# Kernel optimization log

Hardware: AMD Instinct MI355X
Metric: run time of the kernel (lower is better)

Reference implementation:

```python
import jax, jax.numpy as jnp
import numpy as np

N_MENTIONS = 4096
N_PAIRS = 32768
N_SEGMENTS = 1024  # number of spans (ragged softmax groups)
G_DIM = 3 * 768    # span representation dim (3*embed_dim)
D_IN = 3 * G_DIM + 20
HIDDEN = 150


def setup_inputs() -> dict:
    key = jax.random.key(0)
    ks = jax.random.split(key, 11)
    inp = {
        "g_i": jax.random.normal(ks[0], (N_MENTIONS, G_DIM), jnp.float32),
        "mention_scores": jax.random.normal(ks[1], (N_MENTIONS, 1), jnp.float32),
        "speaker_embed": jax.random.normal(ks[2], (3, 20), jnp.float32) * 0.02,
        "W1": jax.random.normal(ks[3], (D_IN, HIDDEN), jnp.float32) * (1.0 / np.sqrt(D_IN)),
        "b1": jnp.zeros((HIDDEN,), jnp.float32),
        "W2": jax.random.normal(ks[4], (HIDDEN, 1), jnp.float32) * (1.0 / np.sqrt(HIDDEN)),
        "b2": jnp.zeros((1,), jnp.float32),
        "mention_ids": jax.random.randint(ks[5], (N_PAIRS,), 0, N_MENTIONS),
        "antecedent_ids": jax.random.randint(ks[6], (N_PAIRS,), 0, N_MENTIONS),
        "speaker_labels": jax.random.randint(ks[7], (N_PAIRS,), 0, 3),
        "segment_ids": jnp.sort(jax.random.randint(ks[8], (N_PAIRS,), 0, N_SEGMENTS)),
    }
    return inp


def reference(g_i, mention_scores, speaker_embed, W1, b1, W2, b2,
              mention_ids, antecedent_ids, speaker_labels, segment_ids):
    # Gather mention / antecedent span representations. [P, G]
    i_g = g_i[mention_ids]
    j_g = g_i[antecedent_ids]
    phi = speaker_embed[speaker_labels]  # [P, speaker_dim]

    # Pair features: cat(i_g, j_g, i_g*j_g, phi). [P, D_IN]
    pairs = jnp.concatenate([i_g, j_g, i_g * j_g, phi], axis=1)

    # Score MLP: Linear -> ReLU -> Linear(->1). (dropout off in eval)
    h = jax.nn.relu(pairs @ W1 + b1)          # [P, HIDDEN]
    s_ij = (h @ W2 + b2)[:, 0]                # [P]

    # coref score = s_i + s_j + s_ij
    s_i = mention_scores[mention_ids, 0]
    s_j = mention_scores[antecedent_ids, 0]
    scores = s_i + s_j + s_ij                 # [P]

    # Ragged per-span softmax with an appended epsilon logit of 0.0.
    seg_max = jax.ops.segment_max(scores, segment_ids, num_segments=N_SEGMENTS)
    m = jnp.maximum(seg_max, 0.0)             # include epsilon=0 in the max
    e = jnp.exp(scores - m[segment_ids])      # [P]
    eps_e = jnp.exp(-m)                       # [S] exp(0 - m)
    denom = jax.ops.segment_sum(e, segment_ids, num_segments=N_SEGMENTS) + eps_e
    pair_probs = e / denom[segment_ids]       # [P]
    eps_probs = eps_e / denom                 # [S]

    # Flattened: all pair probs followed by the per-span epsilon probs.
    return jnp.concatenate([pair_probs, eps_probs])
```

## Files before the change

### kernel.cpp

```cpp
#include <hip/hip_runtime.h>
#include <cstdint>

#define NM   4096
#define NP   32768
#define NSEG 1024
#define GD   2304
#define HID  150
#define NPAD 160
#define KG32 72
#define SEG_ELEMS (KG32 * 10 * 512)

typedef unsigned short u16;
typedef short s16x8 __attribute__((ext_vector_type(8)));
typedef float f32x4 __attribute__((ext_vector_type(4)));
typedef uint32_t u32x4 __attribute__((ext_vector_type(4)));

union Frag {
    uint32_t u[4];
    s16x8    v;
};

__device__ inline uint32_t cvtpk(float lo, float hi) {
    uint32_t r;
    asm("v_cvt_pk_bf16_f32 %0, %1, %2" : "=v"(r) : "v"(lo), "v"(hi));
    return r;
}

__device__ inline f32x4 mfma16(s16x8 a, s16x8 b, f32x4 c) {
    return __builtin_amdgcn_mfma_f32_16x16x32_bf16(a, b, c, 0, 0, 0);
}

__device__ inline s16x8 prodpack(u32x4 iu, u32x4 ju) {
    Frag f;
#pragma unroll
    for (int m = 0; m < 4; ++m) {
        uint32_t x = iu[m], y = ju[m];
        float lo = __builtin_bit_cast(float, x << 16) *
                   __builtin_bit_cast(float, y << 16);
        float hi = __builtin_bit_cast(float, x & 0xffff0000u) *
                   __builtin_bit_cast(float, y & 0xffff0000u);
        f.u[m] = cvtpk(lo, hi);
    }
    return f.v;
}

__global__ void prep_pack_kernel(const float* __restrict__ W1,
                                 u16* __restrict__ wpack,
                                 float* __restrict__ APre) {
    int idx = blockIdx.x * 256 + threadIdx.x;
    if (idx < (NM * 320 / 4))
        ((f32x4*)APre)[idx] = (f32x4){0.f, 0.f, 0.f, 0.f};
    if (idx >= 3 * SEG_ELEMS) return;
    int segi = idx / SEG_ELEMS;
    int t    = idx - segi * SEG_ELEMS;
    int kg   = t / 5120;
    int r    = t - kg * 5120;
    int nf   = r >> 9;
    int q    = r & 511;
    int lane = q >> 3, j = q & 7;
    int kl = kg * 32 + ((lane >> 4) << 3) + j;
    int n  = nf * 16 + (lane & 15);
    int kbase = (segi == 0) ? 2 * GD : ((segi == 1) ? 0 : GD);
    float v = (n < HID) ? W1[(size_t)(kbase + kl) * HID + n] : 0.f;
    uint32_t a = __builtin_bit_cast(uint32_t, v);
    wpack[idx] = (u16)((a + 0x7fffu + ((a >> 16) & 1u)) >> 16);
}

__global__ void prep_tables_kernel(const float* __restrict__ spk,
                                   const float* __restrict__ W1,
                                   const float* __restrict__ b1,
                                   const float* __restrict__ W2,
                                   float* __restrict__ phib,
                                   float* __restrict__ w2pad) {
    int t = threadIdx.x;
    if (t < 3 * NPAD) {
        int s = t / NPAD, n = t - s * NPAD;
        float a = 0.f;
        if (n < HID) {
            for (int d = 0; d < 20; ++d)
                a = fmaf(spk[s * 20 + d], W1[(size_t)(3 * GD + d) * HID + n], a);
            a += b1[n];
        }
        phib[t] = a;
    } else if (t < 4 * NPAD) {
        int n = t - 3 * NPAD;
        w2pad[n] = (n < HID) ? W2[n] : 0.f;
    }
}

struct A2 { f32x4 x0, x1; };

__launch_bounds__(128)
__global__ void gemm_pre_kernel(const float* __restrict__ gi,
                                const u16* __restrict__ wpackIJ,
                                u16* __restrict__ gbf,
                                float* __restrict__ APre) {
    const int tid = threadIdx.x;
    const int wave = tid >> 6, lane = tid & 63;
    const int quad = lane >> 4, l15 = lane & 15;
    const int mt = blockIdx.x, ng = blockIdx.y, ks = blockIdx.z;
    const u16* wp = wpackIJ + (size_t)ng * SEG_ELEMS + lane * 8;
    const int row = mt * 32 + wave * 16 + l15;

    f32x4 acc[10];
#pragma unroll
    for (int b = 0; b < 10; ++b) acc[b] = (f32x4){0.f, 0.f, 0.f, 0.f};

    const float* ap = gi + (size_t)row * GD + quad * 8;
    u16* gb = gbf + (size_t)row * GD + quad * 8;
    const bool emit = (ng == 0);
    const int u0 = ks * 18;

    A2 a0, a1, a2;
    Frag b0[10], b1[10];

#define LDA(ax, k) { ax.x0 = *(const f32x4*)(ap + (u0 + (k)) * 32); \
                     ax.x1 = *(const f32x4*)(ap + (u0 + (k)) * 32 + 4); }
#define LDBP(bb, k) { const u16* wn = wp + (size_t)(u0 + (k)) * 5120; \
        _Pragma("unroll") for (int nf = 0; nf < 10; ++nf) \
            bb[nf].v = *(const s16x8*)(const void*)(wn + nf * 512); }
#define PHP(k, ax, bb) { \
        Frag a; \
        a.u[0] = cvtpk(ax.x0[0], ax.x0[1]); a.u[1] = cvtpk(ax.x0[2], ax.x0[3]); \
        a.u[2] = cvtpk(ax.x1[0], ax.x1[1]); a.u[3] = cvtpk(ax.x1[2], ax.x1[3]); \
        if (emit) *(u32x4*)(gb + (u0 + (k)) * 32) = *(const u32x4*)a.u; \
        _Pragma("unroll") for (int nf = 0; nf < 10; ++nf) \
            acc[nf] = mfma16(a.v, bb[nf].v, acc[nf]); }

    LDA(a0, 0); LDA(a1, 1); LDA(a2, 2);
    LDBP(b0, 0); LDBP(b1, 1);

#pragma unroll 1
    for (int t = 0; t < 2; ++t) {
        const int kb = t * 6;
        PHP(kb + 0, a0, b0); LDA(a0, kb + 3); LDBP(b0, kb + 2);
        PHP(kb + 1, a1, b1); LDA(a1, kb + 4); LDBP(b1, kb + 3);
        PHP(kb + 2, a2, b0); LDA(a2, kb + 5); LDBP(b0, kb + 4);
        PHP(kb + 3, a0, b1); LDA(a0, kb + 6); LDBP(b1, kb + 5);
        PHP(kb + 4, a1, b0); LDA(a1, kb + 7); LDBP(b0, kb + 6);
        PHP(kb + 5, a2, b1); LDA(a2, kb + 8); LDBP(b1, kb + 7);
    }
    PHP(12, a0, b0); LDA(a0, 15); LDBP(b0, 14);
    PHP(13, a1, b1); LDA(a1, 16); LDBP(b1, 15);
    PHP(14, a2, b0); LDA(a2, 17); LDBP(b0, 16);
    PHP(15, a0, b1); LDBP(b1, 17);
    PHP(16, a1, b0);
    PHP(17, a2, b1);

#undef LDA
#undef LDBP
#undef PHP

    const int colbase = ng * NPAD + l15;
    float* Ap = APre + (size_t)(mt * 32 + wave * 16 + quad * 4) * 320 + colbase;
#pragma unroll
    for (int nf = 0; nf < 10; ++nf)
#pragma unroll
        for (int r = 0; r < 4; ++r)
            atomicAdd(&Ap[(size_t)r * 320 + nf * 16], acc[nf][r]);
}

struct G4 { u32x4 i0, j0, i1, j1; };

__launch_bounds__(128)
__global__ void gemm_pairs_kernel(const u16* __restrict__ gbf,
                                  const u16* __restrict__ wpackP,
                                  const float* __restrict__ APre,
                                  const float* __restrict__ phib,
                                  const float* __restrict__ w2pad,
                                  const float* __restrict__ mscore,
                                  const float* __restrict__ b2,
                                  const int* __restrict__ mids,
                                  const int* __restrict__ aids,
                                  const int* __restrict__ slab,
                                  float* __restrict__ scores) {
    const int tid = threadIdx.x;
    const int wave = tid >> 6, lane = tid & 63;
    const int quad = lane >> 4, l15 = lane & 15;
    const int base = blockIdx.x * 64 + wave * 32;

    f32x4 acc[2][10];
#pragma unroll
    for (int a = 0; a < 2; ++a)
#pragma unroll
        for (int b = 0; b < 10; ++b) acc[a][b] = (f32x4){0.f, 0.f, 0.f, 0.f};

    const int p0 = base + l15, p1 = base + 16 + l15;
    const u16* ip0 = gbf + (size_t)mids[p0] * GD + quad * 8;
    const u16* jp0 = gbf + (size_t)aids[p0] * GD + quad * 8;
    const u16* ip1 = gbf + (size_t)mids[p1] * GD + quad * 8;
    const u16* jp1 = gbf + (size_t)aids[p1] * GD + quad * 8;
    const u16* wl = wpackP + lane * 8;

    G4 g0, g1, g2;
    Frag b0[10], b1[10];

#define LDG(g, k) { const int off = (k) * 32; \
        g.i0 = *(const u32x4*)(ip0 + off); g.j0 = *(const u32x4*)(jp0 + off); \
        g.i1 = *(const u32x4*)(ip1 + off); g.j1 = *(const u32x4*)(jp1 + off); }
#define LDB(bb, k) { const u16* wn = wl + (size_t)(k) * 5120; \
        _Pragma("unroll") for (int nf = 0; nf < 10; ++nf) \
            bb[nf].v = *(const s16x8*)(const void*)(wn + nf * 512); }
#define PH(k, g, bb) { \
        s16x8 a0 = prodpack(g.i0, g.j0); \
        s16x8 a1 = prodpack(g.i1, g.j1); \
        _Pragma("unroll") for (int nf = 0; nf < 10; ++nf) { \
            acc[0][nf] = mfma16(a0, bb[nf].v, acc[0][nf]); \
            acc[1][nf] = mfma16(a1, bb[nf].v, acc[1][nf]); } }

    LDG(g0, 0); LDG(g1, 1); LDG(g2, 2);
    LDB(b0, 0); LDB(b1, 1);

#pragma unroll 1
    for (int t = 0; t < 11; ++t) {
        const int kb = t * 6;
        PH(kb + 0, g0, b0); LDG(g0, kb + 3); LDB(b0, kb + 2);
        PH(kb + 1, g1, b1); LDG(g1, kb + 4); LDB(b1, kb + 3);
        PH(kb + 2, g2, b0); LDG(g2, kb + 5); LDB(b0, kb + 4);
        PH(kb + 3, g0, b1); LDG(g0, kb + 6); LDB(b1, kb + 5);
        PH(kb + 4, g1, b0); LDG(g1, kb + 7); LDB(b0, kb + 6);
        PH(kb + 5, g2, b1); LDG(g2, kb + 8); LDB(b1, kb + 7);
    }
    PH(66, g0, b0); LDG(g0, 69); LDB(b0, 68);
    PH(67, g1, b1); LDG(g1, 70); LDB(b1, 69);
    PH(68, g2, b0); LDG(g2, 71); LDB(b0, 70);
    PH(69, g0, b1); LDB(b1, 71);
    PH(70, g1, b0);
    PH(71, g2, b1);

#undef LDG
#undef LDB
#undef PH

    float w2v[10];
#pragma unroll
    for (int nf = 0; nf < 10; ++nf) w2v[nf] = w2pad[nf * 16 + l15];
    const float b2v = b2[0];

#pragma unroll
    for (int mf = 0; mf < 2; ++mf)
#pragma unroll
        for (int r = 0; r < 4; ++r) {
            const int p  = base + mf * 16 + quad * 4 + r;
            const int mi = mids[p], ai = aids[p], sp = slab[p];
            const float* Ai = APre + (size_t)mi * 320;
            const float* Bj = APre + (size_t)ai * 320 + NPAD;
            const float* Ph = phib + sp * NPAD;
            float partial = 0.f;
#pragma unroll
            for (int nf = 0; nf < 10; ++nf) {
                const int c = nf * 16 + l15;
                float h = acc[mf][nf][r] + Ai[c] + Bj[c] + Ph[c];
                h = fmaxf(h, 0.f);
                partial = fmaf(h, w2v[nf], partial);
            }
            partial += __shfl_xor(partial, 1);
            partial += __shfl_xor(partial, 2);
            partial += __shfl_xor(partial, 4);
            partial += __shfl_xor(partial, 8);
            if (l15 == 0)
                scores[p] = partial + b2v + mscore[mi] + mscore[ai];
        }
}

__global__ void seg_softmax_kernel(const float* __restrict__ scores,
                                   const int* __restrict__ seg,
                                   float* __restrict__ out) {
    const int s = blockIdx.x;
    const int lane = threadIdx.x;
    int lo = 0, hi = NP;
    while (lo < hi) { int mid = (lo + hi) >> 1; if (seg[mid] < s) lo = mid + 1; else hi = mid; }
    const int start = lo;
    int lo2 = start, hi2 = NP;
    while (lo2 < hi2) { int mid = (lo2 + hi2) >> 1; if (seg[mid] <= s) lo2 = mid + 1; else hi2 = mid; }
    const int end = lo2;

    float m = 0.f;
    for (int i = start + lane; i < end; i += 64) m = fmaxf(m, scores[i]);
#pragma unroll
    for (int msk = 1; msk < 64; msk <<= 1) m = fmaxf(m, __shfl_xor(m, msk));

    float sum = 0.f;
    for (int i = start + lane; i < end; i += 64) sum += __expf(scores[i] - m);
#pragma unroll
    for (int msk = 1; msk < 64; msk <<= 1) sum += __shfl_xor(sum, msk);

    const float epse = __expf(-m);
    const float inv  = 1.f / (sum + epse);
    for (int i = start + lane; i < end; i += 64) out[i] = __expf(scores[i] - m) * inv;
    if (lane == 0) out[NP + s] = epse * inv;
}

extern "C" void kernel_launch(void* const* d_in, const int* in_sizes, int n_in,
                              void* d_out, int out_size, void* d_ws, size_t ws_size,
                              hipStream_t stream) {
    const float* gi     = (const float*)d_in[0];
    const float* mscore = (const float*)d_in[1];
    const float* spk    = (const float*)d_in[2];
    const float* W1     = (const float*)d_in[3];
    const float* b1     = (const float*)d_in[4];
    const float* W2     = (const float*)d_in[5];
    const float* b2     = (const float*)d_in[6];
    const int*   mids   = (const int*)d_in[7];
    const int*   aids   = (const int*)d_in[8];
    const int*   slab   = (const int*)d_in[9];
    const int*   segs   = (const int*)d_in[10];
    float* out = (float*)d_out;

    char* w = (char*)d_ws;
    u16*   gbf    = (u16*)w;
    u16*   wpack  = (u16*)(w + 18874368);
    float* APre   = (float*)(w + 21086208);
    float* scores = (float*)(w + 26329088);
    float* phib   = (float*)(w + 26460160);
    float* w2pad  = (float*)(w + 26462080);

    prep_pack_kernel<<<dim3((3 * SEG_ELEMS + 255) / 256), dim3(256), 0, stream>>>(W1, wpack, APre);
    prep_tables_kernel<<<dim3(1), dim3(640), 0, stream>>>(spk, W1, b1, W2, phib, w2pad);
    gemm_pre_kernel<<<dim3(128, 2, 4), dim3(128), 0, stream>>>(gi, wpack + SEG_ELEMS, gbf, APre);
    gemm_pairs_kernel<<<dim3(512), dim3(128), 0, stream>>>(gbf, wpack, APre, phib, w2pad,
                                                           mscore, b2, mids, aids, slab, scores);
    seg_softmax_kernel<<<dim3(NSEG), dim3(64), 0, stream>>>(scores, segs, out);
}
```

Baseline: 205.8 us.

## Split K across waves in both GEMMs and reduce partials through LDS

The pre-GEMM drops its grid-level K split with global atomicAdd. Instead, four waves in one block each handle a quarter of K and reduce their partials through shared memory, which also removes the APre zero-fill from the pack kernel. The pairs GEMM doubles its block to four waves, with two waves per 32-pair group each covering half of K, and combines them through LDS before the epilogue. MFMA bursts are wrapped in s_setprio, which adds barrier and LDS traffic in exchange for more waves in flight and shorter per-wave K loops.

```diff
diff --git a/kernel.cpp b/kernel.cpp
--- a/kernel.cpp
+++ b/kernel.cpp
@@ -45,11 +45,8 @@
 }
 
 __global__ void prep_pack_kernel(const float* __restrict__ W1,
-                                 u16* __restrict__ wpack,
-                                 float* __restrict__ APre) {
+                                 u16* __restrict__ wpack) {
     int idx = blockIdx.x * 256 + threadIdx.x;
-    if (idx < (NM * 320 / 4))
-        ((f32x4*)APre)[idx] = (f32x4){0.f, 0.f, 0.f, 0.f};
     if (idx >= 3 * SEG_ELEMS) return;
     int segi = idx / SEG_ELEMS;
     int t    = idx - segi * SEG_ELEMS;
@@ -90,17 +87,19 @@
 
 struct A2 { f32x4 x0, x1; };
 
-__launch_bounds__(128)
+__launch_bounds__(256)
 __global__ void gemm_pre_kernel(const float* __restrict__ gi,
                                 const u16* __restrict__ wpackIJ,
                                 u16* __restrict__ gbf,
                                 float* __restrict__ APre) {
     const int tid = threadIdx.x;
-    const int wave = tid >> 6, lane = tid & 63;
+    const int kh = tid >> 6, lane = tid & 63;
     const int quad = lane >> 4, l15 = lane & 15;
-    const int mt = blockIdx.x, ng = blockIdx.y, ks = blockIdx.z;
+    const int mt = blockIdx.x, ng = blockIdx.y;
     const u16* wp = wpackIJ + (size_t)ng * SEG_ELEMS + lane * 8;
-    const int row = mt * 32 + wave * 16 + l15;
+    const int row = mt * 16 + l15;
+
+    __shared__ float xch[3][64][44];
 
     f32x4 acc[10];
 #pragma unroll
@@ -109,7 +108,7 @@
     const float* ap = gi + (size_t)row * GD + quad * 8;
     u16* gb = gbf + (size_t)row * GD + quad * 8;
     const bool emit = (ng == 0);
-    const int u0 = ks * 18;
+    const int u0 = kh * 18;
 
     A2 a0, a1, a2;
     Frag b0[10], b1[10];
@@ -124,8 +123,10 @@
         a.u[0] = cvtpk(ax.x0[0], ax.x0[1]); a.u[1] = cvtpk(ax.x0[2], ax.x0[3]); \
         a.u[2] = cvtpk(ax.x1[0], ax.x1[1]); a.u[3] = cvtpk(ax.x1[2], ax.x1[3]); \
         if (emit) *(u32x4*)(gb + (u0 + (k)) * 32) = *(const u32x4*)a.u; \
+        __builtin_amdgcn_s_setprio(1); \
         _Pragma("unroll") for (int nf = 0; nf < 10; ++nf) \
-            acc[nf] = mfma16(a.v, bb[nf].v, acc[nf]); }
+            acc[nf] = mfma16(a.v, bb[nf].v, acc[nf]); \
+        __builtin_amdgcn_s_setprio(0); }
 
     LDA(a0, 0); LDA(a1, 1); LDA(a2, 2);
     LDBP(b0, 0); LDBP(b1, 1);
@@ -151,18 +152,34 @@
 #undef LDBP
 #undef PHP
 
-    const int colbase = ng * NPAD + l15;
-    float* Ap = APre + (size_t)(mt * 32 + wave * 16 + quad * 4) * 320 + colbase;
-#pragma unroll
-    for (int nf = 0; nf < 10; ++nf)
-#pragma unroll
-        for (int r = 0; r < 4; ++r)
-            atomicAdd(&Ap[(size_t)r * 320 + nf * 16], acc[nf][r]);
+    if (kh != 0) {
+        float* dst = &xch[kh - 1][lane][0];
+#pragma unroll
+        for (int nf = 0; nf < 10; ++nf)
+            *(f32x4*)(dst + nf * 4) = acc[nf];
+    }
+    __syncthreads();
+    if (kh == 0) {
+#pragma unroll
+        for (int k = 0; k < 3; ++k) {
+            const float* src = &xch[k][lane][0];
+#pragma unroll
+            for (int nf = 0; nf < 10; ++nf)
+                acc[nf] += *(const f32x4*)(src + nf * 4);
+        }
+        const int colbase = ng * NPAD + l15;
+        float* Ap = APre + (size_t)(mt * 16 + quad * 4) * 320 + colbase;
+#pragma unroll
+        for (int nf = 0; nf < 10; ++nf)
+#pragma unroll
+            for (int r = 0; r < 4; ++r)
+                Ap[(size_t)r * 320 + nf * 16] = acc[nf][r];
+    }
 }
 
 struct G4 { u32x4 i0, j0, i1, j1; };
 
-__launch_bounds__(128)
+__launch_bounds__(256)
 __global__ void gemm_pairs_kernel(const u16* __restrict__ gbf,
                                   const u16* __restrict__ wpackP,
                                   const float* __restrict__ APre,
@@ -175,9 +192,12 @@
                                   const int* __restrict__ slab,
                                   float* __restrict__ scores) {
     const int tid = threadIdx.x;
-    const int wave = tid >> 6, lane = tid & 63;
+    const int w = tid >> 6, lane = tid & 63;
+    const int pg = w >> 1, kh = w & 1;
     const int quad = lane >> 4, l15 = lane & 15;
-    const int base = blockIdx.x * 64 + wave * 32;
+    const int base = blockIdx.x * 64 + pg * 32;
+
+    __shared__ float xch[2][64][84];
 
     f32x4 acc[2][10];
 #pragma unroll
@@ -190,12 +210,13 @@
     const u16* jp0 = gbf + (size_t)aids[p0] * GD + quad * 8;
     const u16* ip1 = gbf + (size_t)mids[p1] * GD + quad * 8;
     const u16* jp1 = gbf + (size_t)aids[p1] * GD + quad * 8;
-    const u16* wl = wpackP + lane * 8;
+    const int ko = kh * 36;
+    const u16* wl = wpackP + (size_t)ko * 5120 + lane * 8;
 
     G4 g0, g1, g2;
     Frag b0[10], b1[10];
 
-#define LDG(g, k) { const int off = (k) * 32; \
+#define LDG(g, k) { const int off = (ko + (k)) * 32; \
         g.i0 = *(const u32x4*)(ip0 + off); g.j0 = *(const u32x4*)(jp0 + off); \
         g.i1 = *(const u32x4*)(ip1 + off); g.j1 = *(const u32x4*)(jp1 + off); }
 #define LDB(bb, k) { const u16* wn = wl + (size_t)(k) * 5120; \
@@ -204,15 +225,17 @@
 #define PH(k, g, bb) { \
         s16x8 a0 = prodpack(g.i0, g.j0); \
         s16x8 a1 = prodpack(g.i1, g.j1); \
+        __builtin_amdgcn_s_setprio(1); \
         _Pragma("unroll") for (int nf = 0; nf < 10; ++nf) { \
             acc[0][nf] = mfma16(a0, bb[nf].v, acc[0][nf]); \
-            acc[1][nf] = mfma16(a1, bb[nf].v, acc[1][nf]); } }
+            acc[1][nf] = mfma16(a1, bb[nf].v, acc[1][nf]); } \
+        __builtin_amdgcn_s_setprio(0); }
 
     LDG(g0, 0); LDG(g1, 1); LDG(g2, 2);
     LDB(b0, 0); LDB(b1, 1);
 
 #pragma unroll 1
-    for (int t = 0; t < 11; ++t) {
+    for (int t = 0; t < 5; ++t) {
         const int kb = t * 6;
         PH(kb + 0, g0, b0); LDG(g0, kb + 3); LDB(b0, kb + 2);
         PH(kb + 1, g1, b1); LDG(g1, kb + 4); LDB(b1, kb + 3);
@@ -221,16 +244,36 @@
         PH(kb + 4, g1, b0); LDG(g1, kb + 7); LDB(b0, kb + 6);
         PH(kb + 5, g2, b1); LDG(g2, kb + 8); LDB(b1, kb + 7);
     }
-    PH(66, g0, b0); LDG(g0, 69); LDB(b0, 68);
-    PH(67, g1, b1); LDG(g1, 70); LDB(b1, 69);
-    PH(68, g2, b0); LDG(g2, 71); LDB(b0, 70);
-    PH(69, g0, b1); LDB(b1, 71);
-    PH(70, g1, b0);
-    PH(71, g2, b1);
+    PH(30, g0, b0); LDG(g0, 33); LDB(b0, 32);
+    PH(31, g1, b1); LDG(g1, 34); LDB(b1, 33);
+    PH(32, g2, b0); LDG(g2, 35); LDB(b0, 34);
+    PH(33, g0, b1); LDB(b1, 35);
+    PH(34, g1, b0);
+    PH(35, g2, b1);
 
 #undef LDG
 #undef LDB
 #undef PH
+
+    if (kh == 1) {
+        float* dst = &xch[pg][lane][0];
+#pragma unroll
+        for (int mf = 0; mf < 2; ++mf)
+#pragma unroll
+            for (int nf = 0; nf < 10; ++nf)
+                *(f32x4*)(dst + mf * 40 + nf * 4) = acc[mf][nf];
+    }
+    __syncthreads();
+    if (kh == 1) return;
+
+    {
+        const float* src = &xch[pg][lane][0];
+#pragma unroll
+        for (int mf = 0; mf < 2; ++mf)
+#pragma unroll
+            for (int nf = 0; nf < 10; ++nf)
+                acc[mf][nf] += *(const f32x4*)(src + mf * 40 + nf * 4);
+    }
 
     float w2v[10];
 #pragma unroll
@@ -315,10 +358,10 @@
     float* phib   = (float*)(w + 26460160);
     float* w2pad  = (float*)(w + 26462080);
 
-    prep_pack_kernel<<<dim3((3 * SEG_ELEMS + 255) / 256), dim3(256), 0, stream>>>(W1, wpack, APre);
+    prep_pack_kernel<<<dim3((3 * SEG_ELEMS + 255) / 256), dim3(256), 0, stream>>>(W1, wpack);
     prep_tables_kernel<<<dim3(1), dim3(640), 0, stream>>>(spk, W1, b1, W2, phib, w2pad);
-    gemm_pre_kernel<<<dim3(128, 2, 4), dim3(128), 0, stream>>>(gi, wpack + SEG_ELEMS, gbf, APre);
-    gemm_pairs_kernel<<<dim3(512), dim3(128), 0, stream>>>(gbf, wpack, APre, phib, w2pad,
+    gemm_pre_kernel<<<dim3(256, 2), dim3(256), 0, stream>>>(gi, wpack + SEG_ELEMS, gbf, APre);
+    gemm_pairs_kernel<<<dim3(512), dim3(256), 0, stream>>>(gbf, wpack, APre, phib, w2pad,
                                                            mscore, b2, mids, aids, slab, scores);
     seg_softmax_kernel<<<dim3(NSEG), dim3(64), 0, stream>>>(scores, segs, out);
 }
```

New measurement: 203.5 us. Within noise of the previous version (-1.2%).
